# Performance work log

Hardware: AMD Instinct MI355X
Metric: run time of the kernel (lower is better)

Reference implementation:

```python
import jax, jax.numpy as jnp
import numpy as np

A, T, N_GRID, RBF, F = 128, 2048, 65536, 16, 128
L_DIMS = (1, 3, 5)  # irreps 0e, 1e, 2e


def setup_inputs() -> dict:
    key = jax.random.key(0)
    ks = jax.random.split(key, 16)
    nrm = lambda k, s, sc=1.0: jax.random.normal(k, s, dtype=jnp.float32) * sc
    w_sc = 1.0 / np.sqrt(F).astype(np.float32)
    return {
        "feat0": nrm(ks[0], (A, F, 1)),
        "feat1": nrm(ks[1], (A, F, 3)),
        "feat2": nrm(ks[2], (A, F, 5)),
        "sph0": nrm(ks[3], (A, T, 1)),
        "sph1": nrm(ks[4], (A, T, 3)),
        "sph2": nrm(ks[5], (A, T, 5)),
        "radial_basis_vals": jax.random.uniform(ks[6], (A, T, RBF), dtype=jnp.float32),
        "mlp_w1": nrm(ks[7], (3, F, F), w_sc),
        "mlp_b1": jnp.zeros((3, F), jnp.float32),
        "mlp_w2": nrm(ks[8], (3, F, F), w_sc),
        "mlp_b2": jnp.zeros((3, F), jnp.float32),
        "mlp_w3": nrm(ks[9], (3, F, RBF * F), w_sc),
        "mlp_b3": jnp.zeros((3, RBF * F), jnp.float32),
        "truncated_idx": jax.random.randint(ks[10], (T,), 0, N_GRID, dtype=jnp.int32),
        "N": N_GRID,
    }


def reference(feat0, feat1, feat2, sph0, sph1, sph2, radial_basis_vals,
              mlp_w1, mlp_b1, mlp_w2, mlp_b2, mlp_w3, mlp_b3,
              truncated_idx, N):
    f_dim = feat0.shape[1]
    rbf = radial_basis_vals.shape[-1]
    inv_features = feat0[..., 0]  # (A, F) scalar (0e) channel
    inv_rbf = jnp.asarray(1.0 / np.sqrt(rbf), dtype=feat0.dtype)
    feats = (feat0, feat1, feat2)
    sphs = (sph0, sph1, sph2)
    spatial_features = jnp.zeros((N, f_dim), dtype=feat0.dtype)
    for i in range(3):  # fixed small loop over irrep chunks
        h = jax.nn.silu(inv_features @ mlp_w1[i] + mlp_b1[i])
        h = jax.nn.silu(h @ mlp_w2[i] + mlp_b2[i])
        rbf_to_f = (h @ mlp_w3[i] + mlp_b3[i]).reshape(-1, rbf, f_dim) * inv_rbf  # (A, RBF, F)
        # reduce over atoms n, sph index d, radial index r -> (T, F)
        sparse = jnp.einsum('ntd,nfd,ntr,nrf->tf', sphs[i], feats[i],
                            radial_basis_vals, rbf_to_f)
        spatial_features = spatial_features.at[truncated_idx].add(sparse)
    return spatial_features
```

## Files before the change

### kernel.cpp

```cpp
#include <hip/hip_runtime.h>
#include <hip/hip_bf16.h>
#include <cstdint>
#include <cstddef>

#define A_DIM 128
#define T_DIM 2048
#define F_DIM 128
#define RBF_DIM 16
#define KDD 2048
#define VT_LD 18432
#define NKG 32
#define BT 64

typedef __attribute__((ext_vector_type(8))) short short8;
typedef __attribute__((ext_vector_type(4))) float f32x4;
typedef __attribute__((ext_vector_type(4))) unsigned int u32x4;

__device__ __forceinline__ float silu_f(float x) {
    return x / (1.0f + __expf(-x));
}

__device__ __forceinline__ unsigned short f2bf(float x) {
    union { float f; unsigned u; } v; v.f = x;
    unsigned r = v.u + 0x7FFFu + ((v.u >> 16) & 1u);
    return (unsigned short)(r >> 16);
}

__device__ __forceinline__ void gl_lds16(const void* g, void* l) {
    __builtin_amdgcn_global_load_lds(
        (const __attribute__((address_space(1))) void*)g,
        (__attribute__((address_space(3))) void*)l, 16, 0, 0);
}

__global__ void zero_kernel(float4* __restrict__ p, int n4) {
    const int stride = gridDim.x * blockDim.x;
    const float4 z = {0.f, 0.f, 0.f, 0.f};
    for (int i = blockIdx.x * blockDim.x + threadIdx.x; i < n4; i += stride)
        p[i] = z;
}

__global__ void mlp12_kernel(const float* __restrict__ feat0,
                             const float* __restrict__ w1, const float* __restrict__ b1,
                             const float* __restrict__ w2, const float* __restrict__ b2,
                             float* __restrict__ h2ws) {
    __shared__ float inv_s[4 * F_DIM];
    __shared__ float h_s[4 * F_DIM];
    const int i  = blockIdx.y;
    const int a0 = blockIdx.x * 4;
    const int tid = threadIdx.x;
    const int f  = tid & 127;
    const int la = tid >> 7;

    inv_s[tid] = feat0[(a0 + la) * F_DIM + f];
    __syncthreads();

    const float* w1i = w1 + (size_t)i * F_DIM * F_DIM;
    float x = b1[i * F_DIM + f];
    #pragma unroll 8
    for (int k = 0; k < F_DIM; ++k)
        x = fmaf(inv_s[la * F_DIM + k], w1i[k * F_DIM + f], x);
    h_s[tid] = silu_f(x);
    __syncthreads();

    const float* w2i = w2 + (size_t)i * F_DIM * F_DIM;
    float y = b2[i * F_DIM + f];
    #pragma unroll 8
    for (int k = 0; k < F_DIM; ++k)
        y = fmaf(h_s[la * F_DIM + k], w2i[k * F_DIM + f], y);
    h2ws[((size_t)i * A_DIM + a0 + la) * F_DIM + f] = silu_f(y);
}

__global__ void mlp3_kernel(const float* __restrict__ h2ws,
                            const float* __restrict__ w3, const float* __restrict__ b3,
                            float* __restrict__ rbfws) {
    __shared__ float h2_s[4 * F_DIM];
    const int i  = blockIdx.z;
    const int a0 = blockIdx.x * 4;
    const int c0 = blockIdx.y * 1024;
    const int tid = threadIdx.x;

    for (int j = tid; j < 4 * F_DIM; j += 256)
        h2_s[j] = h2ws[((size_t)i * A_DIM + a0) * F_DIM + j];
    __syncthreads();

    const int c = c0 + tid * 4;
    const float* w3i = w3 + (size_t)i * F_DIM * 2048;
    float val[4][4];
    #pragma unroll
    for (int a = 0; a < 4; ++a) {
        #pragma unroll
        for (int cc = 0; cc < 4; ++cc)
            val[a][cc] = b3[i * 2048 + c + cc];
    }
    for (int k = 0; k < F_DIM; ++k) {
        const float4 w = *reinterpret_cast<const float4*>(&w3i[(size_t)k * 2048 + c]);
        #pragma unroll
        for (int a = 0; a < 4; ++a) {
            const float h = h2_s[a * F_DIM + k];
            val[a][0] = fmaf(h, w.x, val[a][0]);
            val[a][1] = fmaf(h, w.y, val[a][1]);
            val[a][2] = fmaf(h, w.z, val[a][2]);
            val[a][3] = fmaf(h, w.w, val[a][3]);
        }
    }
    const float inv_rbf = 0.25f;
    #pragma unroll
    for (int a = 0; a < 4; ++a) {
        float4 o;
        o.x = val[a][0] * inv_rbf;
        o.y = val[a][1] * inv_rbf;
        o.z = val[a][2] * inv_rbf;
        o.w = val[a][3] * inv_rbf;
        *reinterpret_cast<float4*>(&rbfws[((size_t)i * A_DIM + a0 + a) * 2048 + c]) = o;
    }
}

__global__ void build_vt_kernel(const float* __restrict__ feat0,
                                const float* __restrict__ feat1,
                                const float* __restrict__ feat2,
                                const float* __restrict__ rbfws,
                                unsigned short* __restrict__ Vt) {
    const int n  = blockIdx.x;
    const int dd = blockIdx.y;
    const int f  = threadIdx.x;

    int i, d;
    float fv;
    if (dd == 0)      { i = 0; d = 0;      fv = feat0[n * F_DIM + f]; }
    else if (dd < 4)  { i = 1; d = dd - 1; fv = feat1[(n * F_DIM + f) * 3 + d]; }
    else              { i = 2; d = dd - 4; fv = feat2[(n * F_DIM + f) * 5 + d]; }

    const float* rb = rbfws + ((size_t)(i * A_DIM + n) * RBF_DIM) * F_DIM + f;
    unsigned short* vp = Vt + (size_t)f * VT_LD + (size_t)dd * KDD + n * 16;
    #pragma unroll
    for (int r = 0; r < RBF_DIM; ++r)
        vp[r] = f2bf(fv * rb[(size_t)r * F_DIM]);
}

template<int MODE>
__global__ void __launch_bounds__(256) gemm_kernel(
        const float* __restrict__ sph0, const float* __restrict__ sph1,
        const float* __restrict__ sph2, const float* __restrict__ radial,
        const unsigned short* __restrict__ Vt,
        float* __restrict__ outbuf) {
    __shared__ unsigned short b_s[F_DIM * 64];
    __shared__ float sph_s[4 * BT];

    const int tid  = threadIdx.x;
    const int lane = tid & 63;
    const int w    = tid >> 6;
    const int wr   = w >> 1;
    const int wc   = w & 1;
    const int t0   = blockIdx.x * BT + wr * 32;
    const int n0   = blockIdx.y * 4;
    const int kq   = lane >> 4;
    const int lf   = lane & 15;

    f32x4 rad[2][2][2];
    #pragma unroll
    for (int m = 0; m < 2; ++m) {
        const int t = t0 + 16 * m + lf;
        #pragma unroll
        for (int ks = 0; ks < 2; ++ks) {
            const int n = n0 + 2 * ks + (kq >> 1);
            const float* rp = radial + ((size_t)n * T_DIM + t) * 16 + (kq & 1) * 8;
            rad[m][ks][0] = *reinterpret_cast<const f32x4*>(rp);
            rad[m][ks][1] = *reinterpret_cast<const f32x4*>(rp + 4);
        }
    }

    const int fs_row = tid >> 3;
    const int cs     = (tid & 7) ^ ((tid >> 3) & 7);
    const unsigned short* gsrc0 = Vt + (size_t)fs_row * VT_LD + n0 * 16 + cs * 8;
    const int nn_s = tid >> 6;
    const int tt_s = tid & 63;
    const size_t sph_tbase = (size_t)(n0 + nn_s) * T_DIM + blockIdx.x * BT + tt_s;

    f32x4 acc[2][4];
    #pragma unroll
    for (int m = 0; m < 2; ++m)
        #pragma unroll
        for (int nf = 0; nf < 4; ++nf)
            acc[m][nf] = (f32x4){0.f, 0.f, 0.f, 0.f};

    #pragma unroll 1
    for (int dd = 0; dd < 9; ++dd) {
        const float* sp; int smul, soff;
        if (dd == 0)     { sp = sph0; smul = 1; soff = 0; }
        else if (dd < 4) { sp = sph1; smul = 3; soff = dd - 1; }
        else             { sp = sph2; smul = 5; soff = dd - 4; }

        __syncthreads();

        const size_t koff = (size_t)dd * KDD;
        #pragma unroll
        for (int q = 0; q < 4; ++q) {
            const unsigned short* gp = gsrc0 + koff + (size_t)(q * 32) * VT_LD;
            void* lp = (void*)((char*)b_s + q * 4096 + w * 1024);
            gl_lds16(gp, lp);
        }
        sph_s[tid] = sp[sph_tbase * smul + soff];

        __syncthreads();

        short8 bfr[2][4];
        #pragma unroll
        for (int ks = 0; ks < 2; ++ks) {
            #pragma unroll
            for (int nf = 0; nf < 4; ++nf) {
                const int f = wc * 64 + 16 * nf + lf;
                const int byte = f * 128 + (((ks * 4 + kq) ^ (lf & 7)) * 16);
                bfr[ks][nf] = *reinterpret_cast<const short8*>((const char*)b_s + byte);
            }
        }

        #pragma unroll
        for (int m = 0; m < 2; ++m) {
            #pragma unroll
            for (int ks = 0; ks < 2; ++ks) {
                const float s = sph_s[(2 * ks + (kq >> 1)) * BT + wr * 32 + 16 * m + lf];
                unsigned int d0, d1, d2, d3;
                asm("v_cvt_pk_bf16_f32 %0, %1, %2" : "=v"(d0)
                    : "v"(s * rad[m][ks][0][0]), "v"(s * rad[m][ks][0][1]));
                asm("v_cvt_pk_bf16_f32 %0, %1, %2" : "=v"(d1)
                    : "v"(s * rad[m][ks][0][2]), "v"(s * rad[m][ks][0][3]));
                asm("v_cvt_pk_bf16_f32 %0, %1, %2" : "=v"(d2)
                    : "v"(s * rad[m][ks][1][0]), "v"(s * rad[m][ks][1][1]));
                asm("v_cvt_pk_bf16_f32 %0, %1, %2" : "=v"(d3)
                    : "v"(s * rad[m][ks][1][2]), "v"(s * rad[m][ks][1][3]));
                union { u32x4 u; short8 s8; } au;
                au.u = (u32x4){d0, d1, d2, d3};
                #pragma unroll
                for (int nf = 0; nf < 4; ++nf)
                    acc[m][nf] = __builtin_amdgcn_mfma_f32_16x16x32_bf16(
                        au.s8, bfr[ks][nf], acc[m][nf], 0, 0, 0);
            }
        }
    }

    float* pb = (MODE == 0)
        ? outbuf + (size_t)blockIdx.y * (T_DIM * F_DIM)
        : outbuf;
    #pragma unroll
    for (int m = 0; m < 2; ++m) {
        #pragma unroll
        for (int nf = 0; nf < 4; ++nf) {
            const int f = wc * 64 + 16 * nf + lf;
            #pragma unroll
            for (int reg = 0; reg < 4; ++reg) {
                const int t = t0 + 16 * m + 4 * kq + reg;
                if (MODE == 0)
                    pb[(size_t)t * F_DIM + f] = acc[m][nf][reg];
                else
                    atomicAdd(&pb[(size_t)t * F_DIM + f], acc[m][nf][reg]);
            }
        }
    }
}

__global__ void scatter_sum_kernel(const float* __restrict__ partial,
                                   const int* __restrict__ tidx,
                                   float* __restrict__ out) {
    const int tid = threadIdx.x;
    const int t = blockIdx.x * 2 + (tid >> 7);
    const int f = tid & 127;
    const int g = tidx[t];
    const float* p = partial + (size_t)t * F_DIM + f;
    float s = 0.0f;
    #pragma unroll
    for (int kg = 0; kg < NKG; ++kg)
        s += p[(size_t)kg * (T_DIM * F_DIM)];
    atomicAdd(&out[(size_t)g * F_DIM + f], s);
}

__global__ void scatter_kernel(const float* __restrict__ sparse,
                               const int* __restrict__ tidx,
                               float* __restrict__ out) {
    const int tid = threadIdx.x;
    const int t = blockIdx.x * 2 + (tid >> 7);
    const int f = tid & 127;
    const int g = tidx[t];
    atomicAdd(&out[(size_t)g * F_DIM + f], sparse[(size_t)t * F_DIM + f]);
}

extern "C" void kernel_launch(void* const* d_in, const int* in_sizes, int n_in,
                              void* d_out, int out_size, void* d_ws, size_t ws_size,
                              hipStream_t stream) {
    const float* feat0  = (const float*)d_in[0];
    const float* feat1  = (const float*)d_in[1];
    const float* feat2  = (const float*)d_in[2];
    const float* sph0   = (const float*)d_in[3];
    const float* sph1   = (const float*)d_in[4];
    const float* sph2   = (const float*)d_in[5];
    const float* radial = (const float*)d_in[6];
    const float* w1     = (const float*)d_in[7];
    const float* b1     = (const float*)d_in[8];
    const float* w2     = (const float*)d_in[9];
    const float* b2     = (const float*)d_in[10];
    const float* w3     = (const float*)d_in[11];
    const float* b3     = (const float*)d_in[12];
    const int*   tidx   = (const int*)d_in[13];
    float* out = (float*)d_out;

    float* rbfws  = (float*)d_ws;
    float* h2ws   = rbfws + 3 * A_DIM * RBF_DIM * F_DIM;

    const size_t plain_need =
        (size_t)(3 * A_DIM * RBF_DIM * F_DIM + 3 * A_DIM * F_DIM) * sizeof(float) +
        (size_t)F_DIM * VT_LD * sizeof(unsigned short) +
        (size_t)NKG * T_DIM * F_DIM * sizeof(float);
    const bool plain = (ws_size >= plain_need);

    zero_kernel<<<2048, 256, 0, stream>>>((float4*)out, out_size / 4);

    mlp12_kernel<<<dim3(A_DIM / 4, 3), 512, 0, stream>>>(feat0, w1, b1, w2, b2, h2ws);
    mlp3_kernel<<<dim3(A_DIM / 4, 2, 3), 256, 0, stream>>>(h2ws, w3, b3, rbfws);

    if (plain) {
        unsigned short* Vt = (unsigned short*)(h2ws + 3 * A_DIM * F_DIM);
        float* partial = (float*)(Vt + (size_t)F_DIM * VT_LD);
        build_vt_kernel<<<dim3(A_DIM, 9), 128, 0, stream>>>(feat0, feat1, feat2, rbfws, Vt);
        gemm_kernel<0><<<dim3(T_DIM / BT, A_DIM / 4), 256, 0, stream>>>(
            sph0, sph1, sph2, radial, Vt, partial);
        scatter_sum_kernel<<<dim3(T_DIM / 2), 256, 0, stream>>>(partial, tidx, out);
    } else {
        float* sparse = h2ws + 3 * A_DIM * F_DIM;
        unsigned short* Vt = (unsigned short*)(sparse + T_DIM * F_DIM);
        hipMemsetAsync(sparse, 0, (size_t)T_DIM * F_DIM * sizeof(float), stream);
        build_vt_kernel<<<dim3(A_DIM, 9), 128, 0, stream>>>(feat0, feat1, feat2, rbfws, Vt);
        gemm_kernel<1><<<dim3(T_DIM / BT, A_DIM / 4), 256, 0, stream>>>(
            sph0, sph1, sph2, radial, Vt, sparse);
        scatter_kernel<<<dim3(T_DIM / 2), 256, 0, stream>>>(sparse, tidx, out);
    }
}
```

Before: 70.15 us.

## Fuse MLP stages into one kernel and fold output zeroing into GEMM

Merges the two MLP kernels (layers 1-2 and layer 3) into a single 512-thread kernel. The second hidden activation now stays in shared memory instead of round-tripping through a global workspace, and one launch is removed. The separate output-zeroing kernel is dropped on the main path: each GEMM block clears a slice of the output before its main work, overlapping the memset with compute. The trade-off is that the fused MLP runs with half as many blocks for the third layer, and the GEMM blocks take on extra store traffic.

```diff
diff --git a/kernel.cpp b/kernel.cpp
--- a/kernel.cpp
+++ b/kernel.cpp
@@ -39,12 +39,14 @@
         p[i] = z;
 }
 
-__global__ void mlp12_kernel(const float* __restrict__ feat0,
-                             const float* __restrict__ w1, const float* __restrict__ b1,
-                             const float* __restrict__ w2, const float* __restrict__ b2,
-                             float* __restrict__ h2ws) {
+__global__ void mlp_fused_kernel(const float* __restrict__ feat0,
+                                 const float* __restrict__ w1, const float* __restrict__ b1,
+                                 const float* __restrict__ w2, const float* __restrict__ b2,
+                                 const float* __restrict__ w3, const float* __restrict__ b3,
+                                 float* __restrict__ rbfws) {
     __shared__ float inv_s[4 * F_DIM];
     __shared__ float h_s[4 * F_DIM];
+    __shared__ float h2_s[4 * F_DIM];
     const int i  = blockIdx.y;
     const int a0 = blockIdx.x * 4;
     const int tid = threadIdx.x;
@@ -67,23 +69,10 @@
     #pragma unroll 8
     for (int k = 0; k < F_DIM; ++k)
         y = fmaf(h_s[la * F_DIM + k], w2i[k * F_DIM + f], y);
-    h2ws[((size_t)i * A_DIM + a0 + la) * F_DIM + f] = silu_f(y);
-}
-
-__global__ void mlp3_kernel(const float* __restrict__ h2ws,
-                            const float* __restrict__ w3, const float* __restrict__ b3,
-                            float* __restrict__ rbfws) {
-    __shared__ float h2_s[4 * F_DIM];
-    const int i  = blockIdx.z;
-    const int a0 = blockIdx.x * 4;
-    const int c0 = blockIdx.y * 1024;
-    const int tid = threadIdx.x;
-
-    for (int j = tid; j < 4 * F_DIM; j += 256)
-        h2_s[j] = h2ws[((size_t)i * A_DIM + a0) * F_DIM + j];
+    h2_s[tid] = silu_f(y);
     __syncthreads();
 
-    const int c = c0 + tid * 4;
+    const int c = tid * 4;
     const float* w3i = w3 + (size_t)i * F_DIM * 2048;
     float val[4][4];
     #pragma unroll
@@ -142,7 +131,8 @@
         const float* __restrict__ sph0, const float* __restrict__ sph1,
         const float* __restrict__ sph2, const float* __restrict__ radial,
         const unsigned short* __restrict__ Vt,
-        float* __restrict__ outbuf) {
+        float* __restrict__ outbuf,
+        float* __restrict__ dout, int out_n4) {
     __shared__ unsigned short b_s[F_DIM * 64];
     __shared__ float sph_s[4 * BT];
 
@@ -155,6 +145,17 @@
     const int n0   = blockIdx.y * 4;
     const int kq   = lane >> 4;
     const int lf   = lane & 15;
+
+    if (MODE == 0) {
+        const int bid = blockIdx.y * gridDim.x + blockIdx.x;
+        const float4 z = {0.f, 0.f, 0.f, 0.f};
+        float4* zp = (float4*)dout;
+        #pragma unroll
+        for (int q = 0; q < 8; ++q) {
+            const int idx = bid * 2048 + q * 256 + tid;
+            if (idx < out_n4) zp[idx] = z;
+        }
+    }
 
     f32x4 rad[2][2][2];
     #pragma unroll
@@ -311,25 +312,24 @@
         (size_t)NKG * T_DIM * F_DIM * sizeof(float);
     const bool plain = (ws_size >= plain_need);
 
-    zero_kernel<<<2048, 256, 0, stream>>>((float4*)out, out_size / 4);
-
-    mlp12_kernel<<<dim3(A_DIM / 4, 3), 512, 0, stream>>>(feat0, w1, b1, w2, b2, h2ws);
-    mlp3_kernel<<<dim3(A_DIM / 4, 2, 3), 256, 0, stream>>>(h2ws, w3, b3, rbfws);
+    mlp_fused_kernel<<<dim3(A_DIM / 4, 3), 512, 0, stream>>>(
+        feat0, w1, b1, w2, b2, w3, b3, rbfws);
 
     if (plain) {
         unsigned short* Vt = (unsigned short*)(h2ws + 3 * A_DIM * F_DIM);
         float* partial = (float*)(Vt + (size_t)F_DIM * VT_LD);
         build_vt_kernel<<<dim3(A_DIM, 9), 128, 0, stream>>>(feat0, feat1, feat2, rbfws, Vt);
         gemm_kernel<0><<<dim3(T_DIM / BT, A_DIM / 4), 256, 0, stream>>>(
-            sph0, sph1, sph2, radial, Vt, partial);
+            sph0, sph1, sph2, radial, Vt, partial, out, out_size / 4);
         scatter_sum_kernel<<<dim3(T_DIM / 2), 256, 0, stream>>>(partial, tidx, out);
     } else {
         float* sparse = h2ws + 3 * A_DIM * F_DIM;
         unsigned short* Vt = (unsigned short*)(sparse + T_DIM * F_DIM);
+        zero_kernel<<<2048, 256, 0, stream>>>((float4*)out, out_size / 4);
         hipMemsetAsync(sparse, 0, (size_t)T_DIM * F_DIM * sizeof(float), stream);
         build_vt_kernel<<<dim3(A_DIM, 9), 128, 0, stream>>>(feat0, feat1, feat2, rbfws, Vt);
         gemm_kernel<1><<<dim3(T_DIM / BT, A_DIM / 4), 256, 0, stream>>>(
-            sph0, sph1, sph2, radial, Vt, sparse);
+            sph0, sph1, sph2, radial, Vt, sparse, out, out_size / 4);
         scatter_kernel<<<dim3(T_DIM / 2), 256, 0, stream>>>(sparse, tidx, out);
     }
 }
```

Measured after the change: 63.73 us. 9.2% less time.
